# Optimization experiments

Measured on AMD Instinct MI355X. Metric: run time of the kernel, lower is better.

The kernel has to match this reference:

```python
import jax, jax.numpy as jnp
import numpy as np

G = 64          # voxel grid side
N_IN = 150000   # input points
N_OUT = 150000  # output points
K = 3           # cubic kernel size
CIN = 32
FOUT = 64


def _make_cloud(rng, n):
    flat = rng.permutation(G ** 3)[:n]
    x = flat % G
    y = (flat // G) % G
    z = flat // (G * G)
    pos = np.stack([x, y, z], axis=-1).astype(np.float32) + 0.5  # voxel centers
    return flat, pos


def setup_inputs() -> dict:
    rng = np.random.default_rng(0)
    flat_in, inp_pos = _make_cloud(rng, N_IN)
    _, out_pos = _make_cloud(np.random.default_rng(1), N_OUT)

    # Fixed-radius (Linf, r = K*voxel*0.51 = 1.53) search on the grid ==
    # 3x3x3 voxel neighborhood lookup. Build dense voxel -> point-index map.
    grid = np.full(G ** 3, -1, dtype=np.int64)
    grid[flat_in] = np.arange(N_IN)
    offs = np.stack(np.meshgrid(*([np.arange(-1, 2)] * 3), indexing='ij'), -1).reshape(-1, 3)  # [27,3]
    out_vox = (out_pos - 0.5).astype(np.int64)              # [M,3]
    nb = out_vox[:, None, :] + offs[None, :, :]             # [M,27,3]
    inb = ((nb >= 0) & (nb < G)).all(-1)                    # [M,27]
    flat = nb[..., 0] + G * nb[..., 1] + G * G * nb[..., 2]
    flat = np.where(inb, flat, 0)
    found = grid[flat]
    mask = inb & (found >= 0)
    nbr_idx = np.where(mask, found, 0).astype(np.int32)

    key = jax.random.key(0)
    k1, k2, k3, k4, k5 = jax.random.split(key, 5)
    return {
        'inp_features': jax.random.normal(k1, (N_IN, CIN), jnp.float32),
        'inp_positions': jnp.asarray(inp_pos),
        'out_positions': jnp.asarray(out_pos),
        'voxel_size': jnp.asarray(1.0, jnp.float32),
        'inp_importance': jax.random.uniform(k2, (N_IN,), jnp.float32),
        'kernel': jax.random.uniform(k3, (K, K, K, CIN, FOUT), jnp.float32, -0.05, 0.05),
        'bias': jnp.zeros((FOUT,), jnp.float32) + 0.01 * jax.random.normal(k4, (FOUT,)),
        'neighbor_index': jnp.asarray(nbr_idx),
        'neighbor_mask': jnp.asarray(mask),
    }


def _sparse_conv(inp_features, inp_positions, out_positions, voxel_size,
                 inp_importance, kernel, bias, neighbor_index, neighbor_mask):
    # offset = 0 (odd kernel). extent = kernel_size * voxel_size.
    extent = K * voxel_size
    nbr_pos = inp_positions[neighbor_index]                  # [M,Kn,3]
    rel = nbr_pos - out_positions[:, None, :]                # [M,Kn,3]
    # identity coordinate mapping: normalize to [-1,1] over the extent
    n = 2.0 * rel / extent
    # align_corners=False mapping to filter coords, + offset (=0)
    fcoord = (n * 0.5 + 0.5) * K - 0.5                        # [M,Kn,3] (x,y,z)
    idx = jnp.clip(jnp.round(fcoord).astype(jnp.int32), 0, K - 1)
    # kernel is indexed [z,y,x,cin,cout]; positions are [x,y,z]
    flat_cell = idx[..., 2] * (K * K) + idx[..., 1] * K + idx[..., 0]   # [M,Kn]
    onehot = jax.nn.one_hot(flat_cell, K ** 3, dtype=inp_features.dtype)  # [M,Kn,27]
    w = (inp_importance[neighbor_index] * neighbor_mask.astype(inp_features.dtype))  # [M,Kn]
    feat = inp_features[neighbor_index] * w[..., None]       # [M,Kn,Cin]
    # accumulate neighbor features into their kernel cell, then contract with kernel
    cellfeat = jnp.einsum('mko,mkc->moc', onehot, feat)      # [M,27,Cin]
    wflat = kernel.reshape(K ** 3, CIN, FOUT)
    out = jnp.einsum('moc,ocf->mf', cellfeat, wflat)         # [M,F]
    return out + bias


def reference(inp_features, inp_positions, out_positions, voxel_size,
              inp_importance, kernel, bias, neighbor_index, neighbor_mask):
    return _sparse_conv(inp_features, inp_positions, out_positions, voxel_size,
                        inp_importance, kernel, bias, neighbor_index, neighbor_mask)
```

## Files before the change

kernel.cpp:

```cpp
#include <hip/hip_runtime.h>
#include <hip/hip_bf16.h>

#define CELLS 27
#define CIN   32
#define FOUT  64
#define M_OUT 150000
#define N_INP 150000
#define ZROW  N_INP
#define PPW   32
#define NWAVE ((M_OUT + PPW - 1) / PPW)
#define NBLK  ((NWAVE + 3) / 4)
#define WT_ELEMS (CELLS * CIN * FOUT)
#define WT_BYTES (WT_ELEMS * 2)
#define FB_ROWS  (N_INP + 1)
#define FB_BYTES (FB_ROWS * CIN * 2)

typedef __attribute__((ext_vector_type(4))) float f32x4;
typedef __attribute__((ext_vector_type(8))) short bf16x8;

__device__ __forceinline__ short f2bf(float x) {
    union { __hip_bfloat16 h; short s; } u;
    u.h = __float2bfloat16(x);
    return u.s;
}

__global__ __launch_bounds__(256) void prep_kernel(const float* __restrict__ W,
                                                   const float* __restrict__ feat,
                                                   const float* __restrict__ imp,
                                                   unsigned short* __restrict__ Wt,
                                                   unsigned short* __restrict__ fb) {
    int t = blockIdx.x * 256 + threadIdx.x;
    if (t < FB_ROWS * 4) {
        int i = t >> 2, c = t & 3;
        bf16x8 o = {0, 0, 0, 0, 0, 0, 0, 0};
        if (i < N_INP) {
            float w = imp[i];
            const float* fp = feat + (size_t)i * CIN + c * 8;
            f32x4 f0 = *(const f32x4*)fp;
            f32x4 f1 = *(const f32x4*)(fp + 4);
            o[0] = f2bf(f0.x * w); o[1] = f2bf(f0.y * w);
            o[2] = f2bf(f0.z * w); o[3] = f2bf(f0.w * w);
            o[4] = f2bf(f1.x * w); o[5] = f2bf(f1.y * w);
            o[6] = f2bf(f1.z * w); o[7] = f2bf(f1.w * w);
        }
        *(bf16x8*)(fb + (size_t)i * CIN + c * 8) = o;
    } else {
        int u = t - FB_ROWS * 4;
        if (u < WT_ELEMS) {
            int cell = u >> 11;
            int rem  = u & 2047;
            int cin  = rem >> 6;
            int fout = rem & 63;
            Wt[cell * 2048 + fout * 32 + cin] = (unsigned short)f2bf(W[u]);
        }
    }
}

#define CELL_OF(k) (((k) % 3) * 9 + (((k) / 3) % 3) * 3 + ((k) / 9))

__global__ __launch_bounds__(256) void conv32_kernel(
        const float* __restrict__ opos,
        const float* __restrict__ ipos,
        const int*   __restrict__ nbr,
        const unsigned short* __restrict__ Wt,
        const unsigned short* __restrict__ fb,
        const float* __restrict__ bias,
        float* __restrict__ out) {
    __shared__ int s_idx[4][PPW][28];
    __shared__ int s_vox[4][PPW];

    const int wid  = threadIdx.x >> 6;
    const int lane = threadIdx.x & 63;
    const int wave = blockIdx.x * 4 + wid;
    const int m0   = wave * PPW;

    const int vx0 = (int)ipos[0];
    const int vy0 = (int)ipos[1];
    const int vz0 = (int)ipos[2];

    if (lane < PPW) {
        int m = m0 + lane;
        int vp = -1;
        if (m < M_OUT) {
            vp = ((int)opos[m * 3 + 0] + 1) |
                 (((int)opos[m * 3 + 1] + 1) << 8) |
                 (((int)opos[m * 3 + 2] + 1) << 16);
        }
        s_vox[wid][lane] = vp;
    }
    __syncthreads();

    for (int it = 0; it < 14; ++it) {
        int e = it * 64 + lane;
        if (e < CELLS * PPW) {
            int p = e / CELLS;
            int k = e - p * CELLS;
            int m = m0 + p;
            int id = (m < M_OUT) ? nbr[m * CELLS + k] : 0;
            int ox = k / 9, oy = (k / 3) % 3, oz = k % 3;
            int tgt = (vx0 - ox + 2) | ((vy0 - oy + 2) << 8) | ((vz0 - oz + 2) << 16);
            bool valid = (id != 0) | (s_vox[wid][p] == tgt);
            s_idx[wid][p][k] = valid ? id : ZROW;
        }
    }
    __syncthreads();

    const int g = lane >> 4;
    const int r = lane & 15;

    const unsigned short* fbg = fb + g * 8;
    const unsigned short* wb0 = Wt + r * CIN + g * 8;
    const int* idxr0 = &s_idx[wid][r][0];
    const int* idxr1 = &s_idx[wid][16 + r][0];

    f32x4 acc[8];
#pragma unroll
    for (int i = 0; i < 8; ++i) acc[i] = (f32x4){0.f, 0.f, 0.f, 0.f};

    int    pi0[2], pi1[2];
    bf16x8 pa0[2], pa1[2];
    bf16x8 pb[2][4];

    {
        int a0 = idxr0[0], a1 = idxr1[0];
        int b0 = idxr0[1], b1 = idxr1[1];
        pa0[0] = *(const bf16x8*)(fbg + (size_t)a0 * CIN);
        pa1[0] = *(const bf16x8*)(fbg + (size_t)a1 * CIN);
        pa0[1] = *(const bf16x8*)(fbg + (size_t)b0 * CIN);
        pa1[1] = *(const bf16x8*)(fbg + (size_t)b1 * CIN);
#pragma unroll
        for (int t = 0; t < 4; ++t) {
            pb[0][t] = *(const bf16x8*)(wb0 + CELL_OF(0) * (CIN * FOUT) + t * 16 * CIN);
            pb[1][t] = *(const bf16x8*)(wb0 + CELL_OF(1) * (CIN * FOUT) + t * 16 * CIN);
        }
        pi0[0] = idxr0[2]; pi1[0] = idxr1[2];
        pi0[1] = idxr0[3]; pi1[1] = idxr1[3];
    }

#pragma unroll
    for (int k = 0; k < CELLS; ++k) {
        const int s = k & 1;
#pragma unroll
        for (int t = 0; t < 4; ++t) {
            acc[t]     = __builtin_amdgcn_mfma_f32_16x16x32_bf16(pa0[s], pb[s][t], acc[t],     0, 0, 0);
            acc[4 + t] = __builtin_amdgcn_mfma_f32_16x16x32_bf16(pa1[s], pb[s][t], acc[4 + t], 0, 0, 0);
        }
        if (k + 2 < CELLS) {
            pa0[s] = *(const bf16x8*)(fbg + (size_t)pi0[s] * CIN);
            pa1[s] = *(const bf16x8*)(fbg + (size_t)pi1[s] * CIN);
#pragma unroll
            for (int t = 0; t < 4; ++t)
                pb[s][t] = *(const bf16x8*)(wb0 + CELL_OF(k + 2) * (CIN * FOUT) + t * 16 * CIN);
            if (k + 4 < CELLS) {
                pi0[s] = idxr0[k + 4];
                pi1[s] = idxr1[k + 4];
            }
        }
    }

    float bb0 = bias[r], bb1 = bias[16 + r], bb2 = bias[32 + r], bb3 = bias[48 + r];
#pragma unroll
    for (int frag = 0; frag < 2; ++frag) {
        int base = m0 + frag * 16 + 4 * g;
#pragma unroll
        for (int j = 0; j < 4; ++j) {
            int m = base + j;
            if (m < M_OUT) {
                float* op = out + (size_t)m * FOUT + r;
                op[0]  = acc[frag * 4 + 0][j] + bb0;
                op[16] = acc[frag * 4 + 1][j] + bb1;
                op[32] = acc[frag * 4 + 2][j] + bb2;
                op[48] = acc[frag * 4 + 3][j] + bb3;
            }
        }
    }
}

extern "C" void kernel_launch(void* const* d_in, const int* in_sizes, int n_in,
                              void* d_out, int out_size, void* d_ws, size_t ws_size,
                              hipStream_t stream) {
    const float* feat = (const float*)d_in[0];
    const float* ipos = (const float*)d_in[1];
    const float* opos = (const float*)d_in[2];
    const float* imp  = (const float*)d_in[4];
    const float* W    = (const float*)d_in[5];
    const float* bias = (const float*)d_in[6];
    const int*   nbr  = (const int*)d_in[7];
    unsigned short* Wt = (unsigned short*)d_ws;
    unsigned short* fb = (unsigned short*)((char*)d_ws + WT_BYTES);
    float* out = (float*)d_out;

    int prep_threads = FB_ROWS * 4 + WT_ELEMS;
    hipLaunchKernelGGL(prep_kernel, dim3((prep_threads + 255) / 256), dim3(256),
                       0, stream, W, feat, imp, Wt, fb);
    hipLaunchKernelGGL(conv32_kernel, dim3(NBLK), dim3(256), 0, stream,
                       opos, ipos, nbr, Wt, fb, bias, out);
}
```

Measured before the change: 180.7 us.

## Split output features across wave pairs and drop manual software prefetch

Result: slower. 187.1 us (+3.5%).

```diff
diff --git a/kernel.cpp b/kernel.cpp
--- a/kernel.cpp
+++ b/kernel.cpp
@@ -8,8 +8,8 @@
 #define N_INP 150000
 #define ZROW  N_INP
 #define PPW   32
-#define NWAVE ((M_OUT + PPW - 1) / PPW)
-#define NBLK  ((NWAVE + 3) / 4)
+#define PAIRS ((M_OUT + PPW - 1) / PPW)
+#define NBLK  ((PAIRS + 1) / 2)
 #define WT_ELEMS (CELLS * CIN * FOUT)
 #define WT_BYTES (WT_ELEMS * 2)
 #define FB_ROWS  (N_INP + 1)
@@ -58,7 +58,7 @@
 
 #define CELL_OF(k) (((k) % 3) * 9 + (((k) / 3) % 3) * 3 + ((k) / 9))
 
-__global__ __launch_bounds__(256) void conv32_kernel(
+__global__ __launch_bounds__(256, 8) void conv_fsplit_kernel(
         const float* __restrict__ opos,
         const float* __restrict__ ipos,
         const int*   __restrict__ nbr,
@@ -66,19 +66,21 @@
         const unsigned short* __restrict__ fb,
         const float* __restrict__ bias,
         float* __restrict__ out) {
-    __shared__ int s_idx[4][PPW][28];
-    __shared__ int s_vox[4][PPW];
+    __shared__ int s_idx[2][PPW][28];
+    __shared__ int s_vox[2][PPW];
 
-    const int wid  = threadIdx.x >> 6;
-    const int lane = threadIdx.x & 63;
-    const int wave = blockIdx.x * 4 + wid;
-    const int m0   = wave * PPW;
+    const int wid   = threadIdx.x >> 6;
+    const int lane  = threadIdx.x & 63;
+    const int pslot = wid >> 1;
+    const int fhalf = wid & 1;
+    const int pair  = blockIdx.x * 2 + pslot;
+    const int m0    = pair * PPW;
 
     const int vx0 = (int)ipos[0];
     const int vy0 = (int)ipos[1];
     const int vz0 = (int)ipos[2];
 
-    if (lane < PPW) {
+    if (fhalf == 0 && lane < PPW) {
         int m = m0 + lane;
         int vp = -1;
         if (m < M_OUT) {
@@ -86,12 +88,13 @@
                  (((int)opos[m * 3 + 1] + 1) << 8) |
                  (((int)opos[m * 3 + 2] + 1) << 16);
         }
-        s_vox[wid][lane] = vp;
+        s_vox[pslot][lane] = vp;
     }
     __syncthreads();
 
-    for (int it = 0; it < 14; ++it) {
-        int e = it * 64 + lane;
+#pragma unroll
+    for (int it = 0; it < 7; ++it) {
+        int e = it * 128 + fhalf * 64 + lane;
         if (e < CELLS * PPW) {
             int p = e / CELLS;
             int k = e - p * CELLS;
@@ -99,8 +102,8 @@
             int id = (m < M_OUT) ? nbr[m * CELLS + k] : 0;
             int ox = k / 9, oy = (k / 3) % 3, oz = k % 3;
             int tgt = (vx0 - ox + 2) | ((vy0 - oy + 2) << 8) | ((vz0 - oz + 2) << 16);
-            bool valid = (id != 0) | (s_vox[wid][p] == tgt);
-            s_idx[wid][p][k] = valid ? id : ZROW;
+            bool valid = (id != 0) | (s_vox[pslot][p] == tgt);
+            s_idx[pslot][p][k] = valid ? id : ZROW;
         }
     }
     __syncthreads();
@@ -109,56 +112,32 @@
     const int r = lane & 15;
 
     const unsigned short* fbg = fb + g * 8;
-    const unsigned short* wb0 = Wt + r * CIN + g * 8;
-    const int* idxr0 = &s_idx[wid][r][0];
-    const int* idxr1 = &s_idx[wid][16 + r][0];
+    const unsigned short* wb0 = Wt + (fhalf * 32 + r) * CIN + g * 8;
+    const int* idxr0 = &s_idx[pslot][r][0];
+    const int* idxr1 = &s_idx[pslot][16 + r][0];
 
-    f32x4 acc[8];
+    f32x4 acc[4];
 #pragma unroll
-    for (int i = 0; i < 8; ++i) acc[i] = (f32x4){0.f, 0.f, 0.f, 0.f};
-
-    int    pi0[2], pi1[2];
-    bf16x8 pa0[2], pa1[2];
-    bf16x8 pb[2][4];
-
-    {
-        int a0 = idxr0[0], a1 = idxr1[0];
-        int b0 = idxr0[1], b1 = idxr1[1];
-        pa0[0] = *(const bf16x8*)(fbg + (size_t)a0 * CIN);
-        pa1[0] = *(const bf16x8*)(fbg + (size_t)a1 * CIN);
-        pa0[1] = *(const bf16x8*)(fbg + (size_t)b0 * CIN);
-        pa1[1] = *(const bf16x8*)(fbg + (size_t)b1 * CIN);
-#pragma unroll
-        for (int t = 0; t < 4; ++t) {
-            pb[0][t] = *(const bf16x8*)(wb0 + CELL_OF(0) * (CIN * FOUT) + t * 16 * CIN);
-            pb[1][t] = *(const bf16x8*)(wb0 + CELL_OF(1) * (CIN * FOUT) + t * 16 * CIN);
-        }
-        pi0[0] = idxr0[2]; pi1[0] = idxr1[2];
-        pi0[1] = idxr0[3]; pi1[1] = idxr1[3];
-    }
+    for (int i = 0; i < 4; ++i) acc[i] = (f32x4){0.f, 0.f, 0.f, 0.f};
 
 #pragma unroll
     for (int k = 0; k < CELLS; ++k) {
-        const int s = k & 1;
-#pragma unroll
-        for (int t = 0; t < 4; ++t) {
-            acc[t]     = __builtin_amdgcn_mfma_f32_16x16x32_bf16(pa0[s], pb[s][t], acc[t],     0, 0, 0);
-            acc[4 + t] = __builtin_amdgcn_mfma_f32_16x16x32_bf16(pa1[s], pb[s][t], acc[4 + t], 0, 0, 0);
-        }
-        if (k + 2 < CELLS) {
-            pa0[s] = *(const bf16x8*)(fbg + (size_t)pi0[s] * CIN);
-            pa1[s] = *(const bf16x8*)(fbg + (size_t)pi1[s] * CIN);
-#pragma unroll
-            for (int t = 0; t < 4; ++t)
-                pb[s][t] = *(const bf16x8*)(wb0 + CELL_OF(k + 2) * (CIN * FOUT) + t * 16 * CIN);
-            if (k + 4 < CELLS) {
-                pi0[s] = idxr0[k + 4];
-                pi1[s] = idxr1[k + 4];
-            }
-        }
+        const int cell = CELL_OF(k);
+        int i0 = idxr0[k];
+        int i1 = idxr1[k];
+        bf16x8 a0 = *(const bf16x8*)(fbg + (size_t)i0 * CIN);
+        bf16x8 a1 = *(const bf16x8*)(fbg + (size_t)i1 * CIN);
+        const unsigned short* wb = wb0 + cell * (CIN * FOUT);
+        bf16x8 b0 = *(const bf16x8*)(wb);
+        bf16x8 b1 = *(const bf16x8*)(wb + 16 * CIN);
+        acc[0] = __builtin_amdgcn_mfma_f32_16x16x32_bf16(a0, b0, acc[0], 0, 0, 0);
+        acc[1] = __builtin_amdgcn_mfma_f32_16x16x32_bf16(a0, b1, acc[1], 0, 0, 0);
+        acc[2] = __builtin_amdgcn_mfma_f32_16x16x32_bf16(a1, b0, acc[2], 0, 0, 0);
+        acc[3] = __builtin_amdgcn_mfma_f32_16x16x32_bf16(a1, b1, acc[3], 0, 0, 0);
     }
 
-    float bb0 = bias[r], bb1 = bias[16 + r], bb2 = bias[32 + r], bb3 = bias[48 + r];
+    float bb0 = bias[fhalf * 32 + r];
+    float bb1 = bias[fhalf * 32 + 16 + r];
 #pragma unroll
     for (int frag = 0; frag < 2; ++frag) {
         int base = m0 + frag * 16 + 4 * g;
@@ -166,11 +145,9 @@
         for (int j = 0; j < 4; ++j) {
             int m = base + j;
             if (m < M_OUT) {
-                float* op = out + (size_t)m * FOUT + r;
-                op[0]  = acc[frag * 4 + 0][j] + bb0;
-                op[16] = acc[frag * 4 + 1][j] + bb1;
-                op[32] = acc[frag * 4 + 2][j] + bb2;
-                op[48] = acc[frag * 4 + 3][j] + bb3;
+                float* op = out + (size_t)m * FOUT + fhalf * 32 + r;
+                op[0]  = acc[frag * 2 + 0][j] + bb0;
+                op[16] = acc[frag * 2 + 1][j] + bb1;
             }
         }
     }
@@ -193,6 +170,6 @@
     int prep_threads = FB_ROWS * 4 + WT_ELEMS;
     hipLaunchKernelGGL(prep_kernel, dim3((prep_threads + 255) / 256), dim3(256),
                        0, stream, W, feat, imp, Wt, fb);
-    hipLaunchKernelGGL(conv32_kernel, dim3(NBLK), dim3(256), 0, stream,
+    hipLaunchKernelGGL(conv_fsplit_kernel, dim3(NBLK), dim3(256), 0, stream,
                        opos, ipos, nbr, Wt, fb, bias, out);
 }
```
